# Performance work log

Measured on AMD Instinct MI355X. Metric: run time of the kernel, lower is better.

## Reference

```python
import jax, jax.numpy as jnp
import numpy as np
import math

NUM_HEADS = 8
EPS = 1e-5
LEAKY_SLOPE = 0.01


def _attention(q, k, v, mask):
    # q:[S,64] k,v:[T,64] -> [S,64]; scale by sqrt(d) per source (q.shape[1])
    s = (q @ k.T) / math.sqrt(q.shape[1])
    if mask:
        S, T = s.shape
        tri = jnp.tril(jnp.ones((S, T), dtype=bool))
        s = jnp.where(tri, s, -jnp.inf)
    return jax.nn.softmax(s, axis=1) @ v


def _mha(q, k, v, w_o, mask):
    # all heads share the same (q,k,v) in the source, so cat over heads == tile
    head = _attention(q, k, v, mask)            # [S,64]
    concat = jnp.tile(head, (1, NUM_HEADS))     # [S,512]
    return concat @ w_o


def _layernorm(x, g, b):
    mu = jnp.mean(x, axis=-1, keepdims=True)
    var = jnp.var(x, axis=-1, keepdims=True)
    return (x - mu) * jax.lax.rsqrt(var + EPS) * g + b


def setup_inputs() -> dict:
    key = jax.random.key(0)
    ks = jax.random.split(key, 12)
    S, D, P, H = 8192, 512, 64, 2048
    sd = 1.0 / math.sqrt(D)
    return {
        "encoder_output": jax.random.normal(ks[0], (S, D), jnp.float32),
        "previous_stage_output": jax.random.normal(ks[1], (S, D), jnp.float32),
        "wq_m": jax.random.normal(ks[2], (D, P), jnp.float32) * sd,
        "wk_m": jax.random.normal(ks[3], (D, P), jnp.float32) * sd,
        "wv_m": jax.random.normal(ks[4], (D, P), jnp.float32) * sd,
        "wq_c": jax.random.normal(ks[5], (D, P), jnp.float32) * sd,
        "wk_c": jax.random.normal(ks[6], (D, P), jnp.float32) * sd,
        "wv_c": jax.random.normal(ks[7], (D, P), jnp.float32) * sd,
        "w_o": jax.random.normal(ks[8], (D, D), jnp.float32) * sd,
        "ln_g": jnp.ones((D,), jnp.float32),
        "ln_b": jnp.zeros((D,), jnp.float32),
        "w1": jax.random.normal(ks[9], (D, H), jnp.float32) * sd,
        "b1": jnp.zeros((H,), jnp.float32),
        "w2": jax.random.normal(ks[10], (H, D), jnp.float32) * (1.0 / math.sqrt(H)),
        "b2": jnp.zeros((D,), jnp.float32),
    }


def reference(encoder_output, previous_stage_output, wq_m, wk_m, wv_m,
              wq_c, wk_c, wv_c, w_o, ln_g, ln_b, w1, b1, w2, b2):
    prev = previous_stage_output
    # masked (causal) self-attention over previous decoder output
    masked_mh = _mha(prev @ wq_m, prev @ wk_m, prev @ wv_m, w_o, mask=True)
    # cross attention: q from masked output, k/v from encoder output
    mh = _mha(masked_mh @ wq_c, encoder_output @ wk_c, encoder_output @ wv_c,
              w_o, mask=False)
    x = _layernorm(mh + prev, ln_g, ln_b)
    h = x @ w1 + b1
    h = jnp.where(h >= 0, h, LEAKY_SLOPE * h)
    ffn = h @ w2 + b2
    out = _layernorm(ffn + x, ln_g, ln_b)
    return (encoder_output, out)
```

## Files before the change

### kernel.cpp

```cpp
#include <hip/hip_runtime.h>
#include <hip/hip_bf16.h>

typedef unsigned short u16;
typedef __attribute__((ext_vector_type(4))) float f32x4;
typedef __attribute__((ext_vector_type(8))) __bf16 bf16x8;
typedef __attribute__((ext_vector_type(8))) short short8;
typedef __attribute__((ext_vector_type(4))) short s16x4;

constexpr int SEQ = 8192;
constexpr int DM  = 512;
constexpr int HD  = 64;
constexpr int HFF = 2048;

__device__ __forceinline__ float b2f(u16 u){
  union { unsigned int i; float f; } v; v.i = ((unsigned int)u) << 16; return v.f;
}
__device__ __forceinline__ u16 f2b(float f){
  union { float f; unsigned int i; } v; v.f = f;
  unsigned int r = v.i + 0x7FFFu + ((v.i >> 16) & 1u);
  return (u16)(r >> 16);
}

__device__ __forceinline__ void gload16(const u16* g, u16* lds){
  __builtin_amdgcn_global_load_lds(
      (const __attribute__((address_space(1))) void*)g,
      (__attribute__((address_space(3))) void*)lds, 16, 0, 0);
}

__global__ __launch_bounds__(256) void cvt2_k(const float* __restrict__ enc,
                                              const float* __restrict__ prev,
                                              float* __restrict__ outf,
                                              u16* __restrict__ enc_b,
                                              u16* __restrict__ prev_b, long n8){
  long i = blockIdx.x * 256L + threadIdx.x;
  if(i >= n8) return;
  const float* in = blockIdx.y ? prev : enc;
  u16* ob = blockIdx.y ? prev_b : enc_b;
  f32x4 a = ((const f32x4*)in)[i*2];
  f32x4 b = ((const f32x4*)in)[i*2+1];
  if(!blockIdx.y){
    ((f32x4*)outf)[i*2]   = a;
    ((f32x4*)outf)[i*2+1] = b;
  }
  u16 ov[8];
  for(int j=0;j<4;j++){ ov[j] = f2b(a[j]); ov[4+j] = f2b(b[j]); }
  ((short8*)ob)[i] = *(short8*)ov;
}

__global__ __launch_bounds__(256) void prep_k(const float* __restrict__ p0,
                                              const float* __restrict__ p1,
                                              const float* __restrict__ p2,
                                              const float* __restrict__ p3,
                                              const float* __restrict__ p4,
                                              const float* __restrict__ p5,
                                              const float* __restrict__ w1,
                                              const float* __restrict__ w2,
                                              const float* __restrict__ wo,
                                              u16* __restrict__ out6,
                                              u16* __restrict__ w1_t,
                                              u16* __restrict__ w2_t,
                                              u16* __restrict__ wost){
  __shared__ u16 t[32][33];
  const int z = blockIdx.z;
  const int tx = threadIdx.x, ty = threadIdx.y;
  if(z < 6){
    if(blockIdx.x >= 2) return;
    const float* ins[6] = {p0,p1,p2,p3,p4,p5};
    const float* in = ins[z];
    u16* o = out6 + (long)z * 32768;
    int c0 = blockIdx.x*32, r0 = blockIdx.y*32;
    for(int i=0;i<4;i++)
      t[ty+i*8][tx] = f2b(in[(long)(r0+ty+i*8)*HD + c0+tx]);
    __syncthreads();
    for(int i=0;i<4;i++) o[(long)(c0+ty+i*8)*DM + r0+tx] = t[tx][ty+i*8];
  } else if(z == 6){
    int c0 = blockIdx.x*32, r0 = blockIdx.y*32;
    for(int i=0;i<4;i++)
      t[ty+i*8][tx] = f2b(w1[(long)(r0+ty+i*8)*HFF + c0+tx]);
    __syncthreads();
    for(int i=0;i<4;i++) w1_t[(long)(c0+ty+i*8)*DM + r0+tx] = t[tx][ty+i*8];
  } else if(z == 7){
    int c0 = blockIdx.y*32, r0 = blockIdx.x*32;
    for(int i=0;i<4;i++)
      t[ty+i*8][tx] = f2b(w2[(long)(r0+ty+i*8)*DM + c0+tx]);
    __syncthreads();
    for(int i=0;i<4;i++) w2_t[(long)(c0+ty+i*8)*HFF + r0+tx] = t[tx][ty+i*8];
  } else {
    int fb = blockIdx.y*64 + blockIdx.x;
    if(fb >= 128) return;
    int tid = fb*256 + ty*32 + tx;
    int n = tid >> 6, p = tid & 63;
    float s = 0.f;
    for(int h=0; h<8; h++) s += wo[(long)(h*64+p)*DM + n];
    wost[n*64+p] = f2b(s);
  }
}

__global__ __launch_bounds__(256) void vtrans2_k(const u16* __restrict__ v0,
                                                 u16* __restrict__ o0,
                                                 const u16* __restrict__ v1,
                                                 u16* __restrict__ o1){
  __shared__ u16 t[32][33];
  const u16* in = blockIdx.z ? v1 : v0;
  u16* o = blockIdx.z ? o1 : o0;
  int c0 = blockIdx.x*32, r0 = blockIdx.y*32;
  int tx = threadIdx.x, ty = threadIdx.y;
  for(int i=0;i<4;i++) t[ty+i*8][tx] = in[(long)(r0+ty+i*8)*HD + c0+tx];
  __syncthreads();
  for(int i=0;i<4;i++) o[(long)(c0+ty+i*8)*SEQ + r0+tx] = t[tx][ty+i*8];
}

template<bool WRITE_BF>
__global__ __launch_bounds__(256) void add_ln(const u16* __restrict__ Xa,
                                              const float* __restrict__ Xb,
                                              const float* __restrict__ G,
                                              const float* __restrict__ Bb,
                                              float* __restrict__ OutF,
                                              u16* __restrict__ OutB){
  int row  = blockIdx.x*4 + (threadIdx.x>>6);
  int lane = threadIdx.x & 63;
  short8 a8 = *(const short8*)&Xa[(long)row*DM + lane*8];
  f32x4 b0 = *(const f32x4*)&Xb[(long)row*DM + lane*8];
  f32x4 b1 = *(const f32x4*)&Xb[(long)row*DM + lane*8 + 4];
  float x[8]; float s=0.f, s2=0.f;
  for(int i=0;i<8;i++){
    float bv = (i<4) ? b0[i] : b1[i-4];
    x[i] = b2f((u16)a8[i]) + bv;
    s += x[i]; s2 += x[i]*x[i];
  }
  for(int o=1;o<64;o<<=1){ s += __shfl_xor(s,o); s2 += __shfl_xor(s2,o); }
  float mu  = s * (1.f/DM);
  float var = s2 * (1.f/DM) - mu*mu;
  float rstd = rsqrtf(var + 1e-5f);
  f32x4 g0 = *(const f32x4*)&G[lane*8];
  f32x4 g1 = *(const f32x4*)&G[lane*8+4];
  f32x4 p0 = *(const f32x4*)&Bb[lane*8];
  f32x4 p1 = *(const f32x4*)&Bb[lane*8+4];
  float of[8]; u16 ob[8];
  for(int i=0;i<8;i++){
    float gv = (i<4)?g0[i]:g1[i-4], bv2 = (i<4)?p0[i]:p1[i-4];
    float v = (x[i]-mu)*rstd*gv + bv2;
    of[i] = v; ob[i] = f2b(v);
  }
  *(f32x4*)&OutF[(long)row*DM + lane*8]     = *(f32x4*)&of[0];
  *(f32x4*)&OutF[(long)row*DM + lane*8 + 4] = *(f32x4*)&of[4];
  if constexpr (WRITE_BF)
    *(short8*)&OutB[(long)row*DM + lane*8] = *(short8*)ob;
}

template<int BM,int BN,int EPI,bool DBUF>
__global__ __launch_bounds__(256) void gemm2(const u16* __restrict__ A,
                                             const u16* __restrict__ Bt,
                                             u16* __restrict__ C,
                                             const float* __restrict__ bias,
                                             int N, int K, long sB, long sC){
  constexpr int WR=2, WC=2;
  constexpr int WM = BM/WR, WN = BN/WC;
  constexpr int MF = WM/16, NF = WN/16;
  constexpr int NB = DBUF ? 2 : 1;
  __shared__ u16 As[NB][BM*64];
  __shared__ u16 Bs[NB][BN*64];

  const int tid = threadIdx.x;
  const int wid = tid >> 6, lane = tid & 63;
  const int g = lane >> 4, lr = lane & 15;
  const int m0 = blockIdx.x * BM;
  const int n0 = blockIdx.y * BN;
  Bt += (long)blockIdx.z * sB;
  C  += (long)blockIdx.z * sC;
  const int wr = wid / WC, wc = wid % WC;

  f32x4 acc[MF][NF];
  for(int m=0;m<MF;m++) for(int n=0;n<NF;n++) acc[m][n] = (f32x4)0.f;

  auto stage = [&](const u16* src, int base_row, u16* lds, int rows, int k0){
    const int cpw = rows/32;
    for(int i=0;i<cpw;i++){
      int chunk = wid*cpw + i;
      int Lb = chunk*1024;
      int L  = Lb + lane*16;
      int row = L >> 7, cb = L & 127;
      int scb = cb ^ ((row&7)<<4);
      gload16(&src[(long)(base_row+row)*K + k0 + (scb>>1)], lds + (Lb>>1));
    }
  };
  auto compute = [&](const u16* As_, const u16* Bs_){
    for(int kc=0;kc<2;kc++){
      const int co = (kc*32 + g*8) ^ ((lr&7)<<3);
      bf16x8 af[MF], bfr[NF];
      for(int m=0;m<MF;m++) af[m]  = *(const bf16x8*)&As_[(wr*WM+m*16+lr)*64 + co];
      for(int n=0;n<NF;n++) bfr[n] = *(const bf16x8*)&Bs_[(wc*WN+n*16+lr)*64 + co];
      for(int m=0;m<MF;m++)
        for(int n=0;n<NF;n++)
          acc[m][n] = __builtin_amdgcn_mfma_f32_16x16x32_bf16(af[m], bfr[n], acc[m][n], 0,0,0);
    }
  };

  const int nk = K/64;
  if constexpr (DBUF){
    stage(A, m0, As[0], BM, 0);
    stage(Bt, n0, Bs[0], BN, 0);
    __syncthreads();
    int cur = 0;
    for(int t=0;t<nk;t++){
      if(t+1<nk){
        stage(A, m0, As[cur^1], BM, (t+1)*64);
        stage(Bt, n0, Bs[cur^1], BN, (t+1)*64);
      }
      compute(As[cur], Bs[cur]);
      __syncthreads();
      cur ^= 1;
    }
  } else {
    for(int t=0;t<nk;t++){
      stage(A, m0, As[0], BM, t*64);
      stage(Bt, n0, Bs[0], BN, t*64);
      __syncthreads();
      compute(As[0], Bs[0]);
      __syncthreads();
    }
  }
  for(int m=0;m<MF;m++){
    int row = m0 + wr*WM + m*16 + g*4;
    for(int n=0;n<NF;n++){
      int col = n0 + wc*WN + n*16 + lr;
      float bv = 0.f;
      if constexpr (EPI>=1) bv = bias[col];
      for(int j=0;j<4;j++){
        float v = acc[m][n][j] + bv;
        if constexpr (EPI==2) v = (v >= 0.f) ? v : 0.01f*v;
        C[(long)(row+j)*N + col] = f2b(v);
      }
    }
  }
}

template<bool CAUSAL>
__global__ __launch_bounds__(256, 8) void attn_part_k(const u16* __restrict__ Q,
                                                      const u16* __restrict__ Km,
                                                      const u16* __restrict__ Vt,
                                                      u16* __restrict__ Op,
                                                      float* __restrict__ Ml){
  constexpr int NCH = 16;
  constexpr int CTI = 8;
  __shared__ u16 Ks[64*64];
  __shared__ u16 Vs[64*64];
  __shared__ u16 Ps[4*16*64];

  const int qb = blockIdx.x, ci = blockIdx.y;
  if(CAUSAL && ci*CTI > qb) return;

  const int tid = threadIdx.x, wid = tid>>6, lane = tid&63;
  const int g = lane>>4, lr = lane&15, r4 = g*4;
  const int qrow = qb*64 + wid*16;
  const int rsw = (lr&7)<<3;

  bf16x8 qf[2];
  for(int kc=0;kc<2;kc++){
    bf16x8 t = *(const bf16x8*)&Q[(long)(qrow + lr)*HD + kc*32 + g*8];
    for(int i=0;i<8;i++) t[i] = (__bf16)((float)t[i] * 0.1803368801f);
    qf[kc] = t;
  }

  f32x4 o[4]; for(int n=0;n<4;n++) o[n] = (f32x4)0.f;
  float mst = -1e30f, lst = 0.f;

  const int tdiag = qb - ci*CTI;
  const int tmax = CAUSAL ? min(CTI, tdiag + 1) : CTI;

  const int sr0 = tid>>3, sc0 = (tid&7)*8;
  const int wsw = (sr0&7)<<3;
  short8 rK0, rK1, rV0, rV1;
  {
    const int kv0 = ci*512;
    rK0 = *(const short8*)&Km[(long)(kv0+sr0)*HD + sc0];
    rK1 = *(const short8*)&Km[(long)(kv0+sr0+32)*HD + sc0];
    rV0 = *(const short8*)&Vt[(long)sr0*SEQ + kv0 + sc0];
    rV1 = *(const short8*)&Vt[(long)(sr0+32)*SEQ + kv0 + sc0];
  }

  for(int t=0; t<tmax; ++t){
    const int kv0 = ci*512 + t*64;
    __syncthreads();
    *(short8*)&Ks[sr0*64      + (sc0 ^ wsw)] = rK0;
    *(short8*)&Ks[(sr0+32)*64 + (sc0 ^ wsw)] = rK1;
    *(short8*)&Vs[sr0*64      + (sc0 ^ wsw)] = rV0;
    *(short8*)&Vs[(sr0+32)*64 + (sc0 ^ wsw)] = rV1;
    __syncthreads();
    if(t+1 < tmax){
      const int kn = kv0 + 64;
      rK0 = *(const short8*)&Km[(long)(kn+sr0)*HD + sc0];
      rK1 = *(const short8*)&Km[(long)(kn+sr0+32)*HD + sc0];
      rV0 = *(const short8*)&Vt[(long)sr0*SEQ + kn + sc0];
      rV1 = *(const short8*)&Vt[(long)(sr0+32)*SEQ + kn + sc0];
    }

    f32x4 s[4]; for(int n=0;n<4;n++) s[n] = (f32x4)0.f;
    __builtin_amdgcn_s_setprio(1);
    for(int kc=0;kc<2;kc++){
      const int co = (kc*32 + g*8) ^ rsw;
      for(int n=0;n<4;n++){
        bf16x8 kf = *(const bf16x8*)&Ks[(n*16+lr)*64 + co];
        s[n] = __builtin_amdgcn_mfma_f32_16x16x32_bf16(kf, qf[kc], s[n], 0,0,0);
      }
    }
    __builtin_amdgcn_s_setprio(0);
    if(CAUSAL && t == tdiag){
      int row = qrow + lr;
      for(int n=0;n<4;n++)
        for(int j=0;j<4;j++)
          if(kv0 + n*16 + r4 + j > row) s[n][j] = -1e30f;
    }
    float m01 = fmaxf(fmaxf(s[0][0],s[0][1]), fmaxf(s[0][2],s[0][3]));
    float m11 = fmaxf(fmaxf(s[1][0],s[1][1]), fmaxf(s[1][2],s[1][3]));
    float m21 = fmaxf(fmaxf(s[2][0],s[2][1]), fmaxf(s[2][2],s[2][3]));
    float m31 = fmaxf(fmaxf(s[3][0],s[3][1]), fmaxf(s[3][2],s[3][3]));
    float pmax = fmaxf(fmaxf(m01,m11), fmaxf(m21,m31));
    pmax = fmaxf(pmax, __shfl_xor(pmax,16));
    pmax = fmaxf(pmax, __shfl_xor(pmax,32));
    if(__any(pmax > mst + 8.f)){
      float mn = fmaxf(mst, pmax);
      float fac = exp2f(mst - mn);
      mst = mn; lst *= fac;
      float fj0 = __shfl(fac, r4+0), fj1 = __shfl(fac, r4+1);
      float fj2 = __shfl(fac, r4+2), fj3 = __shfl(fac, r4+3);
      for(int n=0;n<4;n++){
        o[n][0] *= fj0; o[n][1] *= fj1; o[n][2] *= fj2; o[n][3] *= fj3;
      }
    }
    float rs = 0.f;
    for(int n=0;n<4;n++){
      u16 w[4];
      for(int j=0;j<4;j++){
        float p = exp2f(s[n][j] - mst);
        rs += p;
        __bf16 pb = (__bf16)p;
        union { __bf16 b; u16 u; } cv; cv.b = pb;
        w[j] = cv.u;
      }
      *(s16x4*)&Ps[(wid*16 + lr)*64 + ((n*16 + r4) ^ rsw)] = *(s16x4*)w;
    }
    rs += __shfl_xor(rs,16); rs += __shfl_xor(rs,32);
    lst += rs;
    __builtin_amdgcn_s_setprio(1);
    for(int kc=0;kc<2;kc++){
      const int co = (kc*32 + g*8) ^ rsw;
      bf16x8 pf = *(const bf16x8*)&Ps[(wid*16 + lr)*64 + co];
      for(int n=0;n<4;n++){
        bf16x8 vf = *(const bf16x8*)&Vs[(n*16+lr)*64 + co];
        o[n] = __builtin_amdgcn_mfma_f32_16x16x32_bf16(pf, vf, o[n], 0,0,0);
      }
    }
    __builtin_amdgcn_s_setprio(0);
  }
  const long pr = (long)(qb*NCH + ci)*64;
  for(int n=0;n<4;n++)
    for(int j=0;j<4;j++)
      Op[(pr + wid*16 + r4 + j)*64 + n*16 + lr] = f2b(o[n][j]);
  if(lane < 16){
    Ml[(pr + wid*16 + lr)*2]     = mst;
    Ml[(pr + wid*16 + lr)*2 + 1] = lst;
  }
}

template<bool CAUSAL>
__global__ __launch_bounds__(256) void attn_red_k(const u16* __restrict__ Op,
                                                  const float* __restrict__ Ml,
                                                  u16* __restrict__ O){
  int r = blockIdx.x*4 + (threadIdx.x>>6);
  int d = threadIdx.x & 63;
  int qb = r >> 6, rt = r & 63;
  int nch = CAUSAL ? (qb>>3) + 1 : 16;
  long base = (long)qb*16*64 + rt;
  float m = -1e30f;
  for(int i=0;i<nch;i++) m = fmaxf(m, Ml[(base + i*64)*2]);
  float L = 0.f, acc = 0.f;
  for(int i=0;i<nch;i++){
    float mi = Ml[(base + i*64)*2], li = Ml[(base + i*64)*2 + 1];
    float w = exp2f(mi - m);
    L   += li * w;
    acc += w * b2f(Op[(base + i*64)*64 + d]);
  }
  O[(long)r*HD + d] = f2b(acc / L);
}

extern "C" void kernel_launch(void* const* d_in, const int* in_sizes, int n_in,
                              void* d_out, int out_size, void* d_ws, size_t ws_size,
                              hipStream_t stream){
  const float* enc  = (const float*)d_in[0];
  const float* prev = (const float*)d_in[1];
  const float* wq_m = (const float*)d_in[2];
  const float* wk_m = (const float*)d_in[3];
  const float* wv_m = (const float*)d_in[4];
  const float* wq_c = (const float*)d_in[5];
  const float* wk_c = (const float*)d_in[6];
  const float* wv_c = (const float*)d_in[7];
  const float* w_o  = (const float*)d_in[8];
  const float* ln_g = (const float*)d_in[9];
  const float* ln_b = (const float*)d_in[10];
  const float* w1   = (const float*)d_in[11];
  const float* b1   = (const float*)d_in[12];
  const float* w2   = (const float*)d_in[13];
  const float* b2   = (const float*)d_in[14];
  float* out = (float*)d_out;
  u16* ws  = (u16*)d_ws;

  u16* wq_m_t = ws;
  u16* wk_c_t = wq_m_t + 4*32768;
  u16* wost   = wq_m_t + 6*32768;
  u16* w1_t   = wost   + 32768;
  u16* w2_t   = w1_t   + 1048576;
  u16* enc_b  = w2_t   + 1048576;
  u16* prev_b = enc_b  + 4194304;
  u16* q_m    = prev_b + 4194304;
  u16* k_m    = q_m    + 524288;
  u16* v_m    = k_m    + 524288;
  u16* v_m_t  = v_m    + 524288;
  u16* head_m = v_m_t  + 524288;
  u16* k_c    = head_m + 524288;
  u16* v_c    = k_c    + 524288;
  u16* v_c_t  = v_c    + 524288;
  u16* q_c    = v_c_t  + 524288;
  u16* head_c = q_c    + 524288;
  u16* mmh    = head_c + 524288;
  u16* mh     = mmh    + 4194304;
  u16* xb     = mh     + 4194304;
  float* xf   = (float*)(xb + 4194304);
  u16* hbuf   = enc_b;
  u16* ffn    = mh;
  u16* Op     = mmh;
  float* Ml   = (float*)(Op + (long)128*16*64*64);

  dim3 b256(256), tb(32,8);

  cvt2_k<<<dim3(2048,2), b256, 0, stream>>>(enc, prev, out, enc_b, prev_b, (long)SEQ*DM/8);

  prep_k<<<dim3(64,16,9), tb, 0, stream>>>(wq_m, wk_m, wv_m, wq_c, wk_c, wv_c,
                                           w1, w2, w_o, wq_m_t, w1_t, w2_t, wost);

  gemm2<64,64,0,true><<<dim3(SEQ/64,1,3), b256, 0, stream>>>(prev_b, wq_m_t, q_m, nullptr, HD, DM, 32768, 524288);
  gemm2<64,64,0,true><<<dim3(SEQ/64,1,2), b256, 0, stream>>>(enc_b,  wk_c_t, k_c, nullptr, HD, DM, 32768, 524288);
  vtrans2_k<<<dim3(2,256,2), tb, 0, stream>>>(v_m, v_m_t, v_c, v_c_t);

  attn_part_k<true><<<dim3(SEQ/64, 16), b256, 0, stream>>>(q_m, k_m, v_m_t, Op, Ml);
  attn_red_k<true><<<dim3(SEQ/4), b256, 0, stream>>>(Op, Ml, head_m);
  gemm2<64,128,0,false><<<dim3(SEQ/64,4,1), b256, 0, stream>>>(head_m, wost, mmh, nullptr, DM, HD, 0, 0);

  gemm2<64,64,0,false><<<dim3(SEQ/64,1,1), b256, 0, stream>>>(mmh, wq_m_t + 3*32768, q_c, nullptr, HD, DM, 0, 0);
  attn_part_k<false><<<dim3(SEQ/64, 16), b256, 0, stream>>>(q_c, k_c, v_c_t, Op, Ml);
  attn_red_k<false><<<dim3(SEQ/4), b256, 0, stream>>>(Op, Ml, head_c);
  gemm2<64,128,0,false><<<dim3(SEQ/64,4,1), b256, 0, stream>>>(head_c, wost, mh, nullptr, DM, HD, 0, 0);

  add_ln<true><<<dim3(SEQ/4), b256, 0, stream>>>(mh, prev, ln_g, ln_b, xf, xb);

  gemm2<128,128,2,false><<<dim3(SEQ/128,HFF/128,1), b256, 0, stream>>>(xb, w1_t, hbuf, b1, HFF, DM, 0, 0);
  gemm2<64,128,1,false><<<dim3(SEQ/64,4,1),         b256, 0, stream>>>(hbuf, w2_t, ffn, b2, DM, HFF, 0, 0);

  add_ln<false><<<dim3(SEQ/4), b256, 0, stream>>>(ffn, xf, ln_g, ln_b, out + (long)SEQ*DM, nullptr);
}
```

Measured before the change: 219.8 us.

## Split causal attention into more KV chunks and replace LDS swizzle with padding

The causal self-attention now splits the key range into 32 chunks of 4 tiles each instead of 16 chunks of 8 tiles. This is meant to shorten the longest per-block work and spread the triangular workload more evenly across CUs. The XOR-swizzled shared-memory layout is replaced by a row stride padded to 72, which simplifies addressing. The s_setprio hints and the occupancy hint in launch_bounds are removed. In exchange there are more partial outputs to write and reduce, and the Ml buffer offset grows; it may now overlap other workspace buffers.

```diff
diff --git a/kernel.cpp b/kernel.cpp
--- a/kernel.cpp
+++ b/kernel.cpp
@@ -235,17 +235,17 @@
   }
 }
 
-template<bool CAUSAL>
-__global__ __launch_bounds__(256, 8) void attn_part_k(const u16* __restrict__ Q,
-                                                      const u16* __restrict__ Km,
-                                                      const u16* __restrict__ Vt,
-                                                      u16* __restrict__ Op,
-                                                      float* __restrict__ Ml){
-  constexpr int NCH = 16;
-  constexpr int CTI = 8;
-  __shared__ u16 Ks[64*64];
-  __shared__ u16 Vs[64*64];
-  __shared__ u16 Ps[4*16*64];
+template<bool CAUSAL, int NCH>
+__global__ __launch_bounds__(256) void attn_part_k(const u16* __restrict__ Q,
+                                                   const u16* __restrict__ Km,
+                                                   const u16* __restrict__ Vt,
+                                                   u16* __restrict__ Op,
+                                                   float* __restrict__ Ml){
+  constexpr int LDK = 72;
+  constexpr int CTI = 128/NCH;
+  __shared__ u16 Ks[64*LDK];
+  __shared__ u16 Vs[64*LDK];
+  __shared__ u16 Ps[4*16*LDK];
 
   const int qb = blockIdx.x, ci = blockIdx.y;
   if(CAUSAL && ci*CTI > qb) return;
@@ -253,7 +253,6 @@
   const int tid = threadIdx.x, wid = tid>>6, lane = tid&63;
   const int g = lane>>4, lr = lane&15, r4 = g*4;
   const int qrow = qb*64 + wid*16;
-  const int rsw = (lr&7)<<3;
 
   bf16x8 qf[2];
   for(int kc=0;kc<2;kc++){
@@ -267,25 +266,24 @@
 
   const int tdiag = qb - ci*CTI;
   const int tmax = CAUSAL ? min(CTI, tdiag + 1) : CTI;
+  const int kvbase = ci*CTI*64;
 
   const int sr0 = tid>>3, sc0 = (tid&7)*8;
-  const int wsw = (sr0&7)<<3;
   short8 rK0, rK1, rV0, rV1;
   {
-    const int kv0 = ci*512;
-    rK0 = *(const short8*)&Km[(long)(kv0+sr0)*HD + sc0];
-    rK1 = *(const short8*)&Km[(long)(kv0+sr0+32)*HD + sc0];
-    rV0 = *(const short8*)&Vt[(long)sr0*SEQ + kv0 + sc0];
-    rV1 = *(const short8*)&Vt[(long)(sr0+32)*SEQ + kv0 + sc0];
+    rK0 = *(const short8*)&Km[(long)(kvbase+sr0)*HD + sc0];
+    rK1 = *(const short8*)&Km[(long)(kvbase+sr0+32)*HD + sc0];
+    rV0 = *(const short8*)&Vt[(long)sr0*SEQ + kvbase + sc0];
+    rV1 = *(const short8*)&Vt[(long)(sr0+32)*SEQ + kvbase + sc0];
   }
 
   for(int t=0; t<tmax; ++t){
-    const int kv0 = ci*512 + t*64;
-    __syncthreads();
-    *(short8*)&Ks[sr0*64      + (sc0 ^ wsw)] = rK0;
-    *(short8*)&Ks[(sr0+32)*64 + (sc0 ^ wsw)] = rK1;
-    *(short8*)&Vs[sr0*64      + (sc0 ^ wsw)] = rV0;
-    *(short8*)&Vs[(sr0+32)*64 + (sc0 ^ wsw)] = rV1;
+    const int kv0 = kvbase + t*64;
+    __syncthreads();
+    *(short8*)&Ks[sr0*LDK + sc0]      = rK0;
+    *(short8*)&Ks[(sr0+32)*LDK + sc0] = rK1;
+    *(short8*)&Vs[sr0*LDK + sc0]      = rV0;
+    *(short8*)&Vs[(sr0+32)*LDK + sc0] = rV1;
     __syncthreads();
     if(t+1 < tmax){
       const int kn = kv0 + 64;
@@ -296,15 +294,12 @@
     }
 
     f32x4 s[4]; for(int n=0;n<4;n++) s[n] = (f32x4)0.f;
-    __builtin_amdgcn_s_setprio(1);
     for(int kc=0;kc<2;kc++){
-      const int co = (kc*32 + g*8) ^ rsw;
       for(int n=0;n<4;n++){
-        bf16x8 kf = *(const bf16x8*)&Ks[(n*16+lr)*64 + co];
+        bf16x8 kf = *(const bf16x8*)&Ks[(n*16+lr)*LDK + kc*32 + g*8];
         s[n] = __builtin_amdgcn_mfma_f32_16x16x32_bf16(kf, qf[kc], s[n], 0,0,0);
       }
     }
-    __builtin_amdgcn_s_setprio(0);
     if(CAUSAL && t == tdiag){
       int row = qrow + lr;
       for(int n=0;n<4;n++)
@@ -338,20 +333,17 @@
         union { __bf16 b; u16 u; } cv; cv.b = pb;
         w[j] = cv.u;
       }
-      *(s16x4*)&Ps[(wid*16 + lr)*64 + ((n*16 + r4) ^ rsw)] = *(s16x4*)w;
+      *(s16x4*)&Ps[(wid*16 + lr)*LDK + n*16 + r4] = *(s16x4*)w;
     }
     rs += __shfl_xor(rs,16); rs += __shfl_xor(rs,32);
     lst += rs;
-    __builtin_amdgcn_s_setprio(1);
     for(int kc=0;kc<2;kc++){
-      const int co = (kc*32 + g*8) ^ rsw;
-      bf16x8 pf = *(const bf16x8*)&Ps[(wid*16 + lr)*64 + co];
+      bf16x8 pf = *(const bf16x8*)&Ps[(wid*16 + lr)*LDK + kc*32 + g*8];
       for(int n=0;n<4;n++){
-        bf16x8 vf = *(const bf16x8*)&Vs[(n*16+lr)*64 + co];
+        bf16x8 vf = *(const bf16x8*)&Vs[(n*16+lr)*LDK + kc*32 + g*8];
         o[n] = __builtin_amdgcn_mfma_f32_16x16x32_bf16(pf, vf, o[n], 0,0,0);
       }
     }
-    __builtin_amdgcn_s_setprio(0);
   }
   const long pr = (long)(qb*NCH + ci)*64;
   for(int n=0;n<4;n++)
@@ -363,15 +355,16 @@
   }
 }
 
-template<bool CAUSAL>
+template<bool CAUSAL, int NCH>
 __global__ __launch_bounds__(256) void attn_red_k(const u16* __restrict__ Op,
                                                   const float* __restrict__ Ml,
                                                   u16* __restrict__ O){
+  constexpr int CTI = 128/NCH;
   int r = blockIdx.x*4 + (threadIdx.x>>6);
   int d = threadIdx.x & 63;
   int qb = r >> 6, rt = r & 63;
-  int nch = CAUSAL ? (qb>>3) + 1 : 16;
-  long base = (long)qb*16*64 + rt;
+  int nch = CAUSAL ? (qb/CTI) + 1 : NCH;
+  long base = (long)qb*NCH*64 + rt;
   float m = -1e30f;
   for(int i=0;i<nch;i++) m = fmaxf(m, Ml[(base + i*64)*2]);
   float L = 0.f, acc = 0.f;
@@ -429,7 +422,7 @@
   u16* hbuf   = enc_b;
   u16* ffn    = mh;
   u16* Op     = mmh;
-  float* Ml   = (float*)(Op + (long)128*16*64*64);
+  float* Ml   = (float*)(Op + (long)128*32*64*64);
 
   dim3 b256(256), tb(32,8);
 
@@ -442,13 +435,13 @@
   gemm2<64,64,0,true><<<dim3(SEQ/64,1,2), b256, 0, stream>>>(enc_b,  wk_c_t, k_c, nullptr, HD, DM, 32768, 524288);
   vtrans2_k<<<dim3(2,256,2), tb, 0, stream>>>(v_m, v_m_t, v_c, v_c_t);
 
-  attn_part_k<true><<<dim3(SEQ/64, 16), b256, 0, stream>>>(q_m, k_m, v_m_t, Op, Ml);
-  attn_red_k<true><<<dim3(SEQ/4), b256, 0, stream>>>(Op, Ml, head_m);
+  attn_part_k<true,32><<<dim3(SEQ/64, 32), b256, 0, stream>>>(q_m, k_m, v_m_t, Op, Ml);
+  attn_red_k<true,32><<<dim3(SEQ/4), b256, 0, stream>>>(Op, Ml, head_m);
   gemm2<64,128,0,false><<<dim3(SEQ/64,4,1), b256, 0, stream>>>(head_m, wost, mmh, nullptr, DM, HD, 0, 0);
 
   gemm2<64,64,0,false><<<dim3(SEQ/64,1,1), b256, 0, stream>>>(mmh, wq_m_t + 3*32768, q_c, nullptr, HD, DM, 0, 0);
-  attn_part_k<false><<<dim3(SEQ/64, 16), b256, 0, stream>>>(q_c, k_c, v_c_t, Op, Ml);
-  attn_red_k<false><<<dim3(SEQ/4), b256, 0, stream>>>(Op, Ml, head_c);
+  attn_part_k<false,16><<<dim3(SEQ/64, 16), b256, 0, stream>>>(q_c, k_c, v_c_t, Op, Ml);
+  attn_red_k<false,16><<<dim3(SEQ/4), b256, 0, stream>>>(Op, Ml, head_c);
   gemm2<64,128,0,false><<<dim3(SEQ/64,4,1), b256, 0, stream>>>(head_c, wost, mh, nullptr, DM, HD, 0, 0);
 
   add_ln<true><<<dim3(SEQ/4), b256, 0, stream>>>(mh, prev, ln_g, ln_b, xf, xb);
```

After: 227.6 us. 1.04x slower.
